# Optimization experiments

Hardware: AMD Instinct MI355X
Metric: run time of the kernel (lower is better)

The kernel has to match this reference:

```python
import jax, jax.numpy as jnp
import numpy as np

N = 100000      # num_nodes
E = 400000      # num edges
HID = 128       # hidden_channels (== in_channels, memory dim)
OUT = 64        # out_channels (per head)
HEADS = 4
HD = HEADS * OUT  # 256, TransformerConv concat output dim


def _lin(k, fan_in, fan_out):
    return jax.random.normal(k, (fan_in, fan_out), jnp.float32) * 0.02


def setup_inputs() -> dict:
    key = jax.random.key(0)
    ks = jax.random.split(key, 16)
    return {
        "edge_index": jax.random.randint(ks[0], (2, E), 0, N, dtype=jnp.int64),
        "edge_time": jax.random.randint(ks[1], (E, 1), 0, 1000000, dtype=jnp.int64),
        "x": jax.random.normal(ks[2], (N, HID), jnp.float32),
        "memory": jax.random.normal(ks[3], (N, HID), jnp.float32),  # TGN memory table (detached in fwd)
        # TransformerConv params (lin_query / lin_key / lin_value / lin_skip, all with bias)
        "Wq": _lin(ks[4], HID, HD), "bq": jnp.zeros((HD,), jnp.float32),
        "Wk": _lin(ks[5], HID, HD), "bk": jnp.zeros((HD,), jnp.float32),
        "Wv": _lin(ks[6], HID, HD), "bv": jnp.zeros((HD,), jnp.float32),
        "Wskip": _lin(ks[7], HID, HD), "bskip": jnp.zeros((HD,), jnp.float32),
        # rating MLP: Linear(512,128) -> ReLU -> Linear(128,64) -> ReLU -> Linear(64,1)
        "W1": _lin(ks[8], 2 * HD, 128), "b1": jnp.zeros((128,), jnp.float32),
        "W2": _lin(ks[9], 128, 64), "b2": jnp.zeros((64,), jnp.float32),
        "W3": _lin(ks[10], 64, 1), "b3": jnp.zeros((1,), jnp.float32),
    }


def reference(edge_index, edge_time, x, memory,
              Wq, bq, Wk, bk, Wv, bv, Wskip, bskip,
              W1, b1, W2, b2, W3, b3):
    src, dst = edge_index[0], edge_index[1]
    n = x.shape[0]

    # x = memory.detach() + x
    h = memory + x  # [N, HID]

    # TransformerConv (heads=4, concat=True, root_weight=True)
    q = (h @ Wq + bq).reshape(n, HEADS, OUT)
    k = (h @ Wk + bk).reshape(n, HEADS, OUT)
    v = (h @ Wv + bv).reshape(n, HEADS, OUT)

    # per-edge attention scores: messages flow src -> dst, softmax over in-edges of dst
    scores = jnp.sum(q[dst] * k[src], axis=-1) / jnp.sqrt(jnp.float32(OUT))  # [E, H]
    smax = jax.ops.segment_max(scores, dst, num_segments=n)                   # [N, H]
    e = jnp.exp(scores - smax[dst])
    denom = jax.ops.segment_sum(e, dst, num_segments=n)
    alpha = e / (denom[dst] + 1e-16)                                          # [E, H]

    agg = jax.ops.segment_sum(alpha[:, :, None] * v[src], dst, num_segments=n)  # [N, H, OUT]
    out = agg.reshape(n, HD) + (h @ Wskip + bskip)                              # skip connection

    # interaction embeddings + MLP head (dropout inactive at eval)
    inter = jnp.concatenate([out[src], out[dst]], axis=-1)  # [E, 512]
    hdd = jax.nn.relu(inter @ W1 + b1)
    hdd = jax.nn.relu(hdd @ W2 + b2)
    rating = jax.nn.sigmoid(hdd @ W3 + b3) * 4.0 + 1.0
    return rating[:, 0]
```

## Files before the change

kernel.cpp:

```cpp
#include <hip/hip_runtime.h>
#include <math.h>

#define N_NODES 100000
#define N_EDGES 400000
#define HID 128
#define HEADS 4
#define OUT_C 64
#define HD 256
#define SCAN_CHUNK 1024
#define NB_SCAN ((N_NODES + SCAN_CHUNK - 1) / SCAN_CHUNK)

typedef __attribute__((ext_vector_type(8))) short bf16x8;
typedef __attribute__((ext_vector_type(4))) float f32x4;

__device__ __forceinline__ unsigned short fbf(float f) {
    unsigned u = __float_as_uint(f);
    unsigned r = (u + 0x7fffu + ((u >> 16) & 1u)) >> 16;
    return (unsigned short)r;
}
__device__ __forceinline__ float bf2f(unsigned short u) {
    return __uint_as_float(((unsigned)u) << 16);
}

__device__ __forceinline__ void gl_lds16(const void* g, void* l) {
    __builtin_amdgcn_global_load_lds(
        (const __attribute__((address_space(1))) unsigned int*)g,
        (__attribute__((address_space(3))) unsigned int*)l,
        16, 0, 0);
}

__global__ __launch_bounds__(256) void init_zero(int* __restrict__ deg,
                                                 int* __restrict__ cursor) {
    int i = blockIdx.x * 256 + threadIdx.x;
    if (i < N_NODES) { deg[i] = 0; cursor[i] = 0; }
}

__global__ __launch_bounds__(256) void k_deg(const int* __restrict__ ei,
                                             int* __restrict__ deg) {
    int e = blockIdx.x * 256 + threadIdx.x;
    if (e < N_EDGES) atomicAdd(&deg[ei[N_EDGES + e]], 1);
}

__global__ __launch_bounds__(256) void k_scan1(const int* __restrict__ deg,
                                               int* __restrict__ rp,
                                               int* __restrict__ bsum) {
    __shared__ int ts[256];
    int b = blockIdx.x, t = threadIdx.x;
    int base = b * SCAN_CHUNK + t * 4;
    int vv[4];
    int s = 0;
#pragma unroll
    for (int i = 0; i < 4; ++i) {
        int d = (base + i < N_NODES) ? deg[base + i] : 0;
        vv[i] = s;
        s += d;
    }
    ts[t] = s;
    __syncthreads();
    for (int off = 1; off < 256; off <<= 1) {
        int x = (t >= off) ? ts[t - off] : 0;
        __syncthreads();
        ts[t] += x;
        __syncthreads();
    }
    int ex = ts[t] - s;
#pragma unroll
    for (int i = 0; i < 4; ++i)
        if (base + i < N_NODES) rp[base + i] = ex + vv[i];
    if (t == 255) bsum[b] = ts[255];
}

__global__ __launch_bounds__(256) void k_scan2(int* __restrict__ bsum) {
    __shared__ int ts[256];
    int t = threadIdx.x;
    int v = (t < NB_SCAN) ? bsum[t] : 0;
    ts[t] = v;
    __syncthreads();
    for (int off = 1; off < 256; off <<= 1) {
        int x = (t >= off) ? ts[t - off] : 0;
        __syncthreads();
        ts[t] += x;
        __syncthreads();
    }
    if (t < NB_SCAN) bsum[t] = ts[t] - v;
}

__global__ __launch_bounds__(256) void k_bucket(const int* __restrict__ ei,
                                                const int* __restrict__ rp,
                                                const int* __restrict__ bsum,
                                                int* __restrict__ cursor,
                                                int* __restrict__ csr_src,
                                                int* __restrict__ csr_dst,
                                                int* __restrict__ csr_eid) {
    int e = blockIdx.x * 256 + threadIdx.x;
    if (e >= N_EDGES) return;
    int src = ei[e];
    int d   = ei[N_EDGES + e];
    int idx = atomicAdd(&cursor[d], 1);
    int s   = rp[d] + bsum[d >> 10] + idx;
    csr_src[s] = src;
    csr_dst[s] = d;
    csr_eid[s] = e;
}

__global__ __launch_bounds__(256) void pack_all(
    const float* __restrict__ Wq, const float* __restrict__ Wk,
    const float* __restrict__ Wv, const float* __restrict__ Ws,
    const float* __restrict__ W1, const float* __restrict__ W2,
    unsigned short* __restrict__ Wp, unsigned short* __restrict__ Wcp,
    unsigned short* __restrict__ W2p) {
    int i = blockIdx.x * 256 + threadIdx.x;
    int lane = i & 63;
    int q = lane >> 4, c = lane & 15;
    if (i < 16384) {
        int nt = (i >> 6) & 15, kt = (i >> 10) & 3, z = i >> 12;
        const float* W = (z == 0) ? Wq : (z == 1) ? Wk : (z == 2) ? Wv : Ws;
#pragma unroll
        for (int j = 0; j < 8; ++j)
            Wp[i * 8 + j] = fbf(W[(kt * 32 + q * 8 + j) * HD + nt * 16 + c]);
    } else if (i < 24576) {
        int ii = i - 16384;
        int nt = (ii >> 6) & 15, kt = ii >> 10;
        int n = nt * 16 + c;
#pragma unroll
        for (int j = 0; j < 8; ++j) {
            int k = kt * 32 + q * 8 + j;
            float v = (n < 128) ? W1[k * 128 + n] : W1[(k + 256) * 128 + (n - 128)];
            Wcp[ii * 8 + j] = fbf(v);
        }
    } else if (i < 25600) {
        int ii = i - 24576;
        int nt = (ii >> 6) & 3, kt = ii >> 8;
#pragma unroll
        for (int j = 0; j < 8; ++j)
            W2p[ii * 8 + j] = fbf(W2[(kt * 32 + q * 8 + j) * 64 + nt * 16 + c]);
    }
}

__global__ __launch_bounds__(256) void k_pre(const float* __restrict__ x,
                                             const float* __restrict__ mem,
                                             unsigned short* __restrict__ H) {
    int idx = blockIdx.x * 256 + threadIdx.x;
    if (idx >= N_NODES * HID / 8) return;
    const float4* x4 = (const float4*)x;
    const float4* m4 = (const float4*)mem;
    float4 a0 = x4[(size_t)idx * 2],     a1 = x4[(size_t)idx * 2 + 1];
    float4 b0 = m4[(size_t)idx * 2],     b1 = m4[(size_t)idx * 2 + 1];
    bf16x8 hv;
    hv[0] = (short)fbf(a0.x + b0.x); hv[1] = (short)fbf(a0.y + b0.y);
    hv[2] = (short)fbf(a0.z + b0.z); hv[3] = (short)fbf(a0.w + b0.w);
    hv[4] = (short)fbf(a1.x + b1.x); hv[5] = (short)fbf(a1.y + b1.y);
    hv[6] = (short)fbf(a1.z + b1.z); hv[7] = (short)fbf(a1.w + b1.w);
    *(bf16x8*)&H[(size_t)idx * 8] = hv;
}

__global__ __launch_bounds__(256, 4) void gemm4(
    const unsigned short* __restrict__ H,
    const unsigned short* __restrict__ Wp,
    const float* __restrict__ bq, const float* __restrict__ bk,
    const float* __restrict__ bv, const float* __restrict__ bs,
    unsigned short* __restrict__ Q, unsigned short* __restrict__ KV,
    unsigned short* __restrict__ S)
{
    __shared__ __align__(16) short sh[4 * 64 * 68];
    short* As = sh;

    const int t = threadIdx.x;
    const int w = t >> 6, l = t & 63;
    const int q = l >> 4, c = l & 15;
    const int z  = blockIdx.y;
    const int m0 = blockIdx.x * 64;

#pragma unroll
    for (int i = 0; i < 4; ++i) {
        int rbase = w * 16 + i * 4;
        int r  = rbase + (l >> 4);
        int gr = m0 + r; if (gr >= N_NODES) gr = N_NODES - 1;
        int ks = (l & 15) ^ (r & 7);
        gl_lds16(&H[(size_t)gr * HID + ks * 8], &As[rbase * 128]);
    }

    const float* bz = (z == 0) ? bq : (z == 1) ? bk : (z == 2) ? bv : bs;
    float bb[4];
#pragma unroll
    for (int nt = 0; nt < 4; ++nt) bb[nt] = bz[w * 64 + nt * 16 + c];

    f32x4 acc[4][4];
#pragma unroll
    for (int mt = 0; mt < 4; ++mt)
#pragma unroll
        for (int nt = 0; nt < 4; ++nt) acc[mt][nt] = (f32x4){0.f, 0.f, 0.f, 0.f};

    __syncthreads();

#pragma unroll
    for (int kt = 0; kt < 4; ++kt) {
        bf16x8 af[4];
#pragma unroll
        for (int mt = 0; mt < 4; ++mt) {
            int row  = mt * 16 + c;
            int slot = (kt * 4 + q) ^ (row & 7);
            af[mt] = *(const bf16x8*)&As[row * 128 + slot * 8];
        }
#pragma unroll
        for (int nt = 0; nt < 4; ++nt) {
            bf16x8 bw8 = *(const bf16x8*)&Wp[(size_t)(((z * 4 + kt) * 16 + w * 4 + nt) * 64 + l) * 8];
#pragma unroll
            for (int mt = 0; mt < 4; ++mt)
                acc[mt][nt] = __builtin_amdgcn_mfma_f32_16x16x32_bf16(af[mt], bw8, acc[mt][nt], 0, 0, 0);
        }
    }
    __syncthreads();

    short* slab = &sh[w * 64 * 68];
#pragma unroll
    for (int nt = 0; nt < 4; ++nt)
#pragma unroll
        for (int mt = 0; mt < 4; ++mt)
#pragma unroll
            for (int r = 0; r < 4; ++r)
                slab[(mt * 16 + q * 4 + r) * 68 + nt * 16 + c] =
                    (short)fbf(acc[mt][nt][r] + bb[nt]);

    const int srow = l >> 3, schk = l & 7;
    if (z == 1 || z == 2) {
        const int voff = (z == 2) ? 4 : 0;
#pragma unroll
        for (int j = 0; j < 8; ++j) {
            int row = j * 8 + srow;
            int gr  = m0 + row;
            if (gr < N_NODES) {
                const short* sp = &slab[row * 68 + schk * 8];
                size_t base = (size_t)gr * 512 + w * 128 + schk * 16 + voff;
                *(ushort4*)&KV[base]     = *(const ushort4*)sp;
                *(ushort4*)&KV[base + 8] = *(const ushort4*)(sp + 4);
            }
        }
    } else {
        unsigned short* Oz = (z == 0) ? Q : S;
#pragma unroll
        for (int j = 0; j < 8; ++j) {
            int row = j * 8 + srow;
            int gr  = m0 + row;
            if (gr < N_NODES)
                *(bf16x8*)&Oz[(size_t)gr * HD + w * 64 + schk * 8] =
                    *(const bf16x8*)&slab[row * 68 + schk * 8];
        }
    }
}

__global__ __launch_bounds__(256) void k_attn(
    const int* __restrict__ rp, const int* __restrict__ bsum,
    const int* __restrict__ deg, const int* __restrict__ csr_src,
    const unsigned short* __restrict__ Q, const unsigned short* __restrict__ KV,
    const unsigned short* __restrict__ S,
    unsigned short* __restrict__ out)
{
    int node = blockIdx.x * 4 + (threadIdx.x >> 6);
    int l = threadIdx.x & 63;
    if (node >= N_NODES) return;
    int start = rp[node] + bsum[node >> 10];
    int cnt   = deg[node];

    float q0, q1, q2, q3;
    {
        ushort4 u = *(const ushort4*)&Q[(size_t)node * HD + l * 4];
        q0 = bf2f(u.x) * 0.125f; q1 = bf2f(u.y) * 0.125f;
        q2 = bf2f(u.z) * 0.125f; q3 = bf2f(u.w) * 0.125f;
    }

    float d = 0.f;
    float a0 = 0.f, a1 = 0.f, a2 = 0.f, a3 = 0.f;

    int i = 0;
    for (; i + 4 <= cnt; i += 4) {
        int s0 = csr_src[start + i];
        int s1 = csr_src[start + i + 1];
        int s2 = csr_src[start + i + 2];
        int s3 = csr_src[start + i + 3];
        bf16x8 k0 = *(const bf16x8*)&KV[(size_t)s0 * 512 + l * 8];
        bf16x8 k1 = *(const bf16x8*)&KV[(size_t)s1 * 512 + l * 8];
        bf16x8 k2 = *(const bf16x8*)&KV[(size_t)s2 * 512 + l * 8];
        bf16x8 k3 = *(const bf16x8*)&KV[(size_t)s3 * 512 + l * 8];
        float sA = q0 * bf2f((unsigned short)k0[0]) + q1 * bf2f((unsigned short)k0[1])
                 + q2 * bf2f((unsigned short)k0[2]) + q3 * bf2f((unsigned short)k0[3]);
        float sB = q0 * bf2f((unsigned short)k1[0]) + q1 * bf2f((unsigned short)k1[1])
                 + q2 * bf2f((unsigned short)k1[2]) + q3 * bf2f((unsigned short)k1[3]);
        float sC = q0 * bf2f((unsigned short)k2[0]) + q1 * bf2f((unsigned short)k2[1])
                 + q2 * bf2f((unsigned short)k2[2]) + q3 * bf2f((unsigned short)k2[3]);
        float sD = q0 * bf2f((unsigned short)k3[0]) + q1 * bf2f((unsigned short)k3[1])
                 + q2 * bf2f((unsigned short)k3[2]) + q3 * bf2f((unsigned short)k3[3]);
        sA += __shfl_xor(sA, 1); sB += __shfl_xor(sB, 1);
        sC += __shfl_xor(sC, 1); sD += __shfl_xor(sD, 1);
        sA += __shfl_xor(sA, 2); sB += __shfl_xor(sB, 2);
        sC += __shfl_xor(sC, 2); sD += __shfl_xor(sD, 2);
        sA += __shfl_xor(sA, 4); sB += __shfl_xor(sB, 4);
        sC += __shfl_xor(sC, 4); sD += __shfl_xor(sD, 4);
        sA += __shfl_xor(sA, 8); sB += __shfl_xor(sB, 8);
        sC += __shfl_xor(sC, 8); sD += __shfl_xor(sD, 8);
        float eA = __expf(sA), eB = __expf(sB), eC = __expf(sC), eD = __expf(sD);
        d += (eA + eB) + (eC + eD);
        a0 += eA * bf2f((unsigned short)k0[4]) + eB * bf2f((unsigned short)k1[4])
            + eC * bf2f((unsigned short)k2[4]) + eD * bf2f((unsigned short)k3[4]);
        a1 += eA * bf2f((unsigned short)k0[5]) + eB * bf2f((unsigned short)k1[5])
            + eC * bf2f((unsigned short)k2[5]) + eD * bf2f((unsigned short)k3[5]);
        a2 += eA * bf2f((unsigned short)k0[6]) + eB * bf2f((unsigned short)k1[6])
            + eC * bf2f((unsigned short)k2[6]) + eD * bf2f((unsigned short)k3[6]);
        a3 += eA * bf2f((unsigned short)k0[7]) + eB * bf2f((unsigned short)k1[7])
            + eC * bf2f((unsigned short)k2[7]) + eD * bf2f((unsigned short)k3[7]);
    }
    for (; i < cnt; ++i) {
        int s0 = csr_src[start + i];
        bf16x8 k0 = *(const bf16x8*)&KV[(size_t)s0 * 512 + l * 8];
        float sA = q0 * bf2f((unsigned short)k0[0]) + q1 * bf2f((unsigned short)k0[1])
                 + q2 * bf2f((unsigned short)k0[2]) + q3 * bf2f((unsigned short)k0[3]);
        sA += __shfl_xor(sA, 1);
        sA += __shfl_xor(sA, 2);
        sA += __shfl_xor(sA, 4);
        sA += __shfl_xor(sA, 8);
        float eA = __expf(sA);
        d += eA;
        a0 += eA * bf2f((unsigned short)k0[4]);
        a1 += eA * bf2f((unsigned short)k0[5]);
        a2 += eA * bf2f((unsigned short)k0[6]);
        a3 += eA * bf2f((unsigned short)k0[7]);
    }

    float inv = 1.f / (d + 1e-16f);
    ushort4 su = *(const ushort4*)&S[(size_t)node * HD + l * 4];
    ushort4 ov = make_ushort4(fbf(bf2f(su.x) + a0 * inv),
                              fbf(bf2f(su.y) + a1 * inv),
                              fbf(bf2f(su.z) + a2 * inv),
                              fbf(bf2f(su.w) + a3 * inv));
    *(ushort4*)&out[(size_t)node * HD + l * 4] = ov;
}

__global__ __launch_bounds__(256, 4) void pd_gemm(
    const unsigned short* __restrict__ outb,
    const unsigned short* __restrict__ Wcp,
    unsigned short* __restrict__ PD)
{
    __shared__ __align__(16) short sh[4 * 64 * 68];
    short* As = sh;

    const int t = threadIdx.x;
    const int w = t >> 6, l = t & 63;
    const int q = l >> 4, c = l & 15;
    const int m0 = blockIdx.x * 64;

#pragma unroll
    for (int i = 0; i < 8; ++i) {
        int rbase = w * 16 + i * 2;
        int r  = rbase + (l >> 5);
        int gr = m0 + r; if (gr >= N_NODES) gr = N_NODES - 1;
        int s  = (l & 31) ^ (r & 7);
        gl_lds16(&outb[(size_t)gr * HD + s * 8], &As[rbase * 256]);
    }

    f32x4 acc[4][4];
#pragma unroll
    for (int mt = 0; mt < 4; ++mt)
#pragma unroll
        for (int nt = 0; nt < 4; ++nt) acc[mt][nt] = (f32x4){0.f, 0.f, 0.f, 0.f};

    __syncthreads();

#pragma unroll
    for (int kt = 0; kt < 8; ++kt) {
        bf16x8 af[4];
#pragma unroll
        for (int mt = 0; mt < 4; ++mt) {
            int row  = mt * 16 + c;
            int slot = (kt * 4 + q) ^ (row & 7);
            af[mt] = *(const bf16x8*)&As[row * 256 + slot * 8];
        }
#pragma unroll
        for (int nt = 0; nt < 4; ++nt) {
            int ntg = w * 4 + nt;
            bf16x8 bv8 = *(const bf16x8*)&Wcp[(size_t)((kt * 16 + ntg) * 64 + l) * 8];
#pragma unroll
            for (int mt = 0; mt < 4; ++mt)
                acc[mt][nt] = __builtin_amdgcn_mfma_f32_16x16x32_bf16(af[mt], bv8, acc[mt][nt], 0, 0, 0);
        }
    }
    __syncthreads();

    short* slab = &sh[w * 64 * 68];
#pragma unroll
    for (int nt = 0; nt < 4; ++nt)
#pragma unroll
        for (int mt = 0; mt < 4; ++mt)
#pragma unroll
            for (int r = 0; r < 4; ++r)
                slab[(mt * 16 + q * 4 + r) * 68 + nt * 16 + c] =
                    (short)fbf(acc[mt][nt][r]);
    const int srow = l >> 3, schk = l & 7;
#pragma unroll
    for (int j = 0; j < 8; ++j) {
        int row = j * 8 + srow;
        int gr = m0 + row;
        if (gr < N_NODES)
            *(bf16x8*)&PD[(size_t)gr * HD + w * 64 + schk * 8] =
                *(const bf16x8*)&slab[row * 68 + schk * 8];
    }
}

__global__ __launch_bounds__(256) void edge_mlp_pd(
    const int* __restrict__ csr_src, const int* __restrict__ csr_dst,
    const int* __restrict__ csr_eid,
    const unsigned short* __restrict__ PD,
    const float* __restrict__ b1,
    const unsigned short* __restrict__ W2p, const float* __restrict__ b2,
    const float* __restrict__ W3, const float* __restrict__ b3,
    float* __restrict__ rating)
{
    __shared__ __align__(16) char lds[64 * 136 * 2];
    short* h1t = (short*)lds;
    float* h2s = (float*)lds;

    const int t = threadIdx.x;
    const int w = t >> 6, l = t & 63;
    const int q = l >> 4, c = l & 15;
    const int e0 = blockIdx.x * 64;

#pragma unroll
    for (int j = 0; j < 4; ++j) {
        int idx = t + j * 256;
        int row = idx >> 4, ch = idx & 15;
        int src = csr_src[e0 + row];
        int dst = csr_dst[e0 + row];
        bf16x8 pv = *(const bf16x8*)&PD[(size_t)src * HD + ch * 8];
        bf16x8 dv = *(const bf16x8*)&PD[(size_t)dst * HD + 128 + ch * 8];
        float4 ba = *(const float4*)&b1[ch * 8];
        float4 bb = *(const float4*)&b1[ch * 8 + 4];
        bf16x8 hv;
        hv[0] = (short)fbf(fmaxf(bf2f((unsigned short)pv[0]) + bf2f((unsigned short)dv[0]) + ba.x, 0.f));
        hv[1] = (short)fbf(fmaxf(bf2f((unsigned short)pv[1]) + bf2f((unsigned short)dv[1]) + ba.y, 0.f));
        hv[2] = (short)fbf(fmaxf(bf2f((unsigned short)pv[2]) + bf2f((unsigned short)dv[2]) + ba.z, 0.f));
        hv[3] = (short)fbf(fmaxf(bf2f((unsigned short)pv[3]) + bf2f((unsigned short)dv[3]) + ba.w, 0.f));
        hv[4] = (short)fbf(fmaxf(bf2f((unsigned short)pv[4]) + bf2f((unsigned short)dv[4]) + bb.x, 0.f));
        hv[5] = (short)fbf(fmaxf(bf2f((unsigned short)pv[5]) + bf2f((unsigned short)dv[5]) + bb.y, 0.f));
        hv[6] = (short)fbf(fmaxf(bf2f((unsigned short)pv[6]) + bf2f((unsigned short)dv[6]) + bb.z, 0.f));
        hv[7] = (short)fbf(fmaxf(bf2f((unsigned short)pv[7]) + bf2f((unsigned short)dv[7]) + bb.w, 0.f));
        *(bf16x8*)&h1t[row * 136 + ch * 8] = hv;
    }
    __syncthreads();

    f32x4 acc2[4];
#pragma unroll
    for (int i = 0; i < 4; ++i) acc2[i] = (f32x4){0.f, 0.f, 0.f, 0.f};
#pragma unroll
    for (int kt = 0; kt < 4; ++kt) {
        bf16x8 av = *(const bf16x8*)&h1t[(w * 16 + c) * 136 + kt * 32 + q * 8];
#pragma unroll
        for (int nt = 0; nt < 4; ++nt) {
            bf16x8 bv = *(const bf16x8*)&W2p[(size_t)((kt * 4 + nt) * 64 + l) * 8];
            acc2[nt] = __builtin_amdgcn_mfma_f32_16x16x32_bf16(av, bv, acc2[nt], 0, 0, 0);
        }
    }
    __syncthreads();

#pragma unroll
    for (int nt = 0; nt < 4; ++nt) {
        float bv = b2[nt * 16 + c];
#pragma unroll
        for (int r = 0; r < 4; ++r)
            h2s[(w * 16 + q * 4 + r) * 65 + nt * 16 + c] = fmaxf(acc2[nt][r] + bv, 0.f);
    }
    __syncthreads();

    if (t < 64) {
        float a = b3[0];
#pragma unroll 8
        for (int kk = 0; kk < 64; ++kk)
            a += h2s[t * 65 + kk] * W3[kk];
        rating[csr_eid[e0 + t]] = 4.f / (1.f + __expf(-a)) + 1.f;
    }
}

extern "C" void kernel_launch(void* const* d_in, const int* in_sizes, int n_in,
                              void* d_out, int out_size, void* d_ws, size_t ws_size,
                              hipStream_t stream) {
    const int*   ei  = (const int*)d_in[0];
    const float* x   = (const float*)d_in[2];
    const float* mem = (const float*)d_in[3];
    const float* Wq  = (const float*)d_in[4];
    const float* bq  = (const float*)d_in[5];
    const float* Wk  = (const float*)d_in[6];
    const float* bk  = (const float*)d_in[7];
    const float* Wv  = (const float*)d_in[8];
    const float* bv  = (const float*)d_in[9];
    const float* Ws  = (const float*)d_in[10];
    const float* bs  = (const float*)d_in[11];
    const float* W1  = (const float*)d_in[12];
    const float* b1  = (const float*)d_in[13];
    const float* W2  = (const float*)d_in[14];
    const float* b2  = (const float*)d_in[15];
    const float* W3  = (const float*)d_in[16];
    const float* b3  = (const float*)d_in[17];
    float* rating = (float*)d_out;

    unsigned short* Q = (unsigned short*)d_ws;
    const size_t NHDe = (size_t)N_NODES * HD;
    unsigned short* KV = Q + NHDe;
    unsigned short* S  = KV + 2 * NHDe;
    unsigned short* H  = S + NHDe;
    int* rp      = (int*)(H + (size_t)N_NODES * HID);
    int* deg     = rp + N_NODES;
    int* cursor  = deg + N_NODES;
    int* csr_src = cursor + N_NODES;
    int* csr_dst = csr_src + N_EDGES;
    int* csr_eid = csr_dst + N_EDGES;
    int* bsum    = csr_eid + N_EDGES;
    unsigned short* Wp  = (unsigned short*)(bsum + 128);
    unsigned short* Wcp = Wp + 16384 * 8;
    unsigned short* W2p = Wcp + 8192 * 8;
    unsigned short* PD  = KV;

    const int nblk  = (N_NODES + 255) / 256;
    const int eblk  = (N_EDGES + 255) / 256;
    const int wgrid = (N_NODES + 3) / 4;
    const int pblk  = (N_NODES * HID / 8 + 255) / 256;

    init_zero<<<nblk, 256, 0, stream>>>(deg, cursor);
    k_deg<<<eblk, 256, 0, stream>>>(ei, deg);
    k_scan1<<<NB_SCAN, 256, 0, stream>>>(deg, rp, bsum);
    k_scan2<<<1, 256, 0, stream>>>(bsum);
    k_bucket<<<eblk, 256, 0, stream>>>(ei, rp, bsum, cursor, csr_src, csr_dst, csr_eid);
    pack_all<<<100, 256, 0, stream>>>(Wq, Wk, Wv, Ws, W1, W2, Wp, Wcp, W2p);

    k_pre<<<pblk, 256, 0, stream>>>(x, mem, H);

    gemm4<<<dim3((N_NODES + 63) / 64, 4), dim3(256), 0, stream>>>(
        H, Wp, bq, bk, bv, bs, Q, KV, S);

    k_attn<<<wgrid, 256, 0, stream>>>(rp, bsum, deg, csr_src, Q, KV, S, Q);

    pd_gemm<<<(N_NODES + 63) / 64, 256, 0, stream>>>(Q, Wcp, PD);

    edge_mlp_pd<<<N_EDGES / 64, 256, 0, stream>>>(
        csr_src, csr_dst, csr_eid, PD, b1, W2p, b2, W3, b3, rating);
}
```

Before: 456.3 us.

## Compute two projections per GEMM block, interleave K/V writes, tweak attention tail

```diff
diff --git a/kernel.cpp b/kernel.cpp
--- a/kernel.cpp
+++ b/kernel.cpp
@@ -9,6 +9,7 @@
 #define HD 256
 #define SCAN_CHUNK 1024
 #define NB_SCAN ((N_NODES + SCAN_CHUNK - 1) / SCAN_CHUNK)
+#define SLAB_STRIDE 4356
 
 typedef __attribute__((ext_vector_type(8))) short bf16x8;
 typedef __attribute__((ext_vector_type(4))) float f32x4;
@@ -27,12 +28,6 @@
         (const __attribute__((address_space(1))) unsigned int*)g,
         (__attribute__((address_space(3))) unsigned int*)l,
         16, 0, 0);
-}
-
-__global__ __launch_bounds__(256) void init_zero(int* __restrict__ deg,
-                                                 int* __restrict__ cursor) {
-    int i = blockIdx.x * 256 + threadIdx.x;
-    if (i < N_NODES) { deg[i] = 0; cursor[i] = 0; }
 }
 
 __global__ __launch_bounds__(256) void k_deg(const int* __restrict__ ei,
@@ -154,7 +149,57 @@
     *(bf16x8*)&H[(size_t)idx * 8] = hv;
 }
 
-__global__ __launch_bounds__(256, 4) void gemm4(
+__device__ __forceinline__ void mfma_pass(f32x4 acc[4][4], const short* As,
+        const unsigned short* __restrict__ Wp, int z, int w, int l, int q, int c) {
+#pragma unroll
+    for (int mt = 0; mt < 4; ++mt)
+#pragma unroll
+        for (int nt = 0; nt < 4; ++nt) acc[mt][nt] = (f32x4){0.f, 0.f, 0.f, 0.f};
+#pragma unroll
+    for (int kt = 0; kt < 4; ++kt) {
+        bf16x8 af[4];
+#pragma unroll
+        for (int mt = 0; mt < 4; ++mt) {
+            int row  = mt * 16 + c;
+            int slot = (kt * 4 + q) ^ (row & 7);
+            af[mt] = *(const bf16x8*)&As[row * 128 + slot * 8];
+        }
+#pragma unroll
+        for (int nt = 0; nt < 4; ++nt) {
+            bf16x8 bw8 = *(const bf16x8*)&Wp[(size_t)(((z * 4 + kt) * 16 + w * 4 + nt) * 64 + l) * 8];
+#pragma unroll
+            for (int mt = 0; mt < 4; ++mt)
+                acc[mt][nt] = __builtin_amdgcn_mfma_f32_16x16x32_bf16(af[mt], bw8, acc[mt][nt], 0, 0, 0);
+        }
+    }
+}
+
+__device__ __forceinline__ void slab_store(short* slab, const f32x4 acc[4][4],
+        const float bb[4], int q, int c) {
+#pragma unroll
+    for (int nt = 0; nt < 4; ++nt)
+#pragma unroll
+        for (int mt = 0; mt < 4; ++mt)
+#pragma unroll
+            for (int r = 0; r < 4; ++r)
+                slab[(mt * 16 + q * 4 + r) * 68 + nt * 16 + c] =
+                    (short)fbf(acc[mt][nt][r] + bb[nt]);
+}
+
+__device__ __forceinline__ void store_rows(unsigned short* __restrict__ O,
+        const short* slab, int m0, int w, int l) {
+    const int srow = l >> 3, schk = l & 7;
+#pragma unroll
+    for (int j = 0; j < 8; ++j) {
+        int row = j * 8 + srow;
+        int gr  = m0 + row;
+        if (gr < N_NODES)
+            *(bf16x8*)&O[(size_t)gr * HD + w * 64 + schk * 8] =
+                *(const bf16x8*)&slab[row * 68 + schk * 8];
+    }
+}
+
+__global__ __launch_bounds__(256, 3) void gemm4(
     const unsigned short* __restrict__ H,
     const unsigned short* __restrict__ Wp,
     const float* __restrict__ bq, const float* __restrict__ bk,
@@ -162,13 +207,13 @@
     unsigned short* __restrict__ Q, unsigned short* __restrict__ KV,
     unsigned short* __restrict__ S)
 {
-    __shared__ __align__(16) short sh[4 * 64 * 68];
-    short* As = sh;
+    __shared__ __align__(16) short As[64 * 128];
+    __shared__ __align__(16) short Slab[4 * SLAB_STRIDE];
 
     const int t = threadIdx.x;
     const int w = t >> 6, l = t & 63;
     const int q = l >> 4, c = l & 15;
-    const int z  = blockIdx.y;
+    const int y  = blockIdx.y;
     const int m0 = blockIdx.x * 64;
 
 #pragma unroll
@@ -180,71 +225,55 @@
         gl_lds16(&H[(size_t)gr * HID + ks * 8], &As[rbase * 128]);
     }
 
-    const float* bz = (z == 0) ? bq : (z == 1) ? bk : (z == 2) ? bv : bs;
-    float bb[4];
-#pragma unroll
-    for (int nt = 0; nt < 4; ++nt) bb[nt] = bz[w * 64 + nt * 16 + c];
-
+    const int   zA  = (y == 0) ? 0 : 1;
+    const int   zB  = (y == 0) ? 3 : 2;
+    const float* bA = (y == 0) ? bq : bk;
+    const float* bB = (y == 0) ? bs : bv;
+    float bbA[4], bbB[4];
+#pragma unroll
+    for (int nt = 0; nt < 4; ++nt) {
+        bbA[nt] = bA[w * 64 + nt * 16 + c];
+        bbB[nt] = bB[w * 64 + nt * 16 + c];
+    }
+
+    __syncthreads();
+
+    short* slab = &Slab[w * SLAB_STRIDE];
     f32x4 acc[4][4];
-#pragma unroll
-    for (int mt = 0; mt < 4; ++mt)
-#pragma unroll
-        for (int nt = 0; nt < 4; ++nt) acc[mt][nt] = (f32x4){0.f, 0.f, 0.f, 0.f};
-
-    __syncthreads();
-
-#pragma unroll
-    for (int kt = 0; kt < 4; ++kt) {
-        bf16x8 af[4];
-#pragma unroll
-        for (int mt = 0; mt < 4; ++mt) {
-            int row  = mt * 16 + c;
-            int slot = (kt * 4 + q) ^ (row & 7);
-            af[mt] = *(const bf16x8*)&As[row * 128 + slot * 8];
-        }
-#pragma unroll
-        for (int nt = 0; nt < 4; ++nt) {
-            bf16x8 bw8 = *(const bf16x8*)&Wp[(size_t)(((z * 4 + kt) * 16 + w * 4 + nt) * 64 + l) * 8];
-#pragma unroll
-            for (int mt = 0; mt < 4; ++mt)
-                acc[mt][nt] = __builtin_amdgcn_mfma_f32_16x16x32_bf16(af[mt], bw8, acc[mt][nt], 0, 0, 0);
-        }
-    }
-    __syncthreads();
-
-    short* slab = &sh[w * 64 * 68];
-#pragma unroll
-    for (int nt = 0; nt < 4; ++nt)
-#pragma unroll
-        for (int mt = 0; mt < 4; ++mt)
-#pragma unroll
-            for (int r = 0; r < 4; ++r)
-                slab[(mt * 16 + q * 4 + r) * 68 + nt * 16 + c] =
-                    (short)fbf(acc[mt][nt][r] + bb[nt]);
-
-    const int srow = l >> 3, schk = l & 7;
-    if (z == 1 || z == 2) {
-        const int voff = (z == 2) ? 4 : 0;
-#pragma unroll
-        for (int j = 0; j < 8; ++j) {
-            int row = j * 8 + srow;
-            int gr  = m0 + row;
+    ushort4 kreg[16];
+    const int koff = (l & 15) * 4;
+    const short* cslab = &Slab[(l >> 4) * SLAB_STRIDE];
+
+    mfma_pass(acc, As, Wp, zA, w, l, q, c);
+    slab_store(slab, acc, bbA, q, c);
+    if (y == 0) {
+        store_rows(Q, slab, m0, w, l);
+    } else {
+        __syncthreads();
+#pragma unroll
+        for (int i = 0; i < 16; ++i)
+            kreg[i] = *(const ushort4*)&cslab[(w * 16 + i) * 68 + koff];
+        __syncthreads();
+    }
+
+    mfma_pass(acc, As, Wp, zB, w, l, q, c);
+    slab_store(slab, acc, bbB, q, c);
+    if (y == 0) {
+        store_rows(S, slab, m0, w, l);
+    } else {
+        __syncthreads();
+#pragma unroll
+        for (int i = 0; i < 16; ++i) {
+            int gr = m0 + w * 16 + i;
+            ushort4 vr = *(const ushort4*)&cslab[(w * 16 + i) * 68 + koff];
             if (gr < N_NODES) {
-                const short* sp = &slab[row * 68 + schk * 8];
-                size_t base = (size_t)gr * 512 + w * 128 + schk * 16 + voff;
-                *(ushort4*)&KV[base]     = *(const ushort4*)sp;
-                *(ushort4*)&KV[base + 8] = *(const ushort4*)(sp + 4);
+                bf16x8 ov;
+                ov[0] = (short)kreg[i].x; ov[1] = (short)kreg[i].y;
+                ov[2] = (short)kreg[i].z; ov[3] = (short)kreg[i].w;
+                ov[4] = (short)vr.x;      ov[5] = (short)vr.y;
+                ov[6] = (short)vr.z;      ov[7] = (short)vr.w;
+                *(bf16x8*)&KV[(size_t)gr * 512 + l * 8] = ov;
             }
-        }
-    } else {
-        unsigned short* Oz = (z == 0) ? Q : S;
-#pragma unroll
-        for (int j = 0; j < 8; ++j) {
-            int row = j * 8 + srow;
-            int gr  = m0 + row;
-            if (gr < N_NODES)
-                *(bf16x8*)&Oz[(size_t)gr * HD + w * 64 + schk * 8] =
-                    *(const bf16x8*)&slab[row * 68 + schk * 8];
         }
     }
 }
@@ -309,7 +338,28 @@
         a3 += eA * bf2f((unsigned short)k0[7]) + eB * bf2f((unsigned short)k1[7])
             + eC * bf2f((unsigned short)k2[7]) + eD * bf2f((unsigned short)k3[7]);
     }
-    for (; i < cnt; ++i) {
+    if (i + 2 <= cnt) {
+        int s0 = csr_src[start + i];
+        int s1 = csr_src[start + i + 1];
+        bf16x8 k0 = *(const bf16x8*)&KV[(size_t)s0 * 512 + l * 8];
+        bf16x8 k1 = *(const bf16x8*)&KV[(size_t)s1 * 512 + l * 8];
+        float sA = q0 * bf2f((unsigned short)k0[0]) + q1 * bf2f((unsigned short)k0[1])
+                 + q2 * bf2f((unsigned short)k0[2]) + q3 * bf2f((unsigned short)k0[3]);
+        float sB = q0 * bf2f((unsigned short)k1[0]) + q1 * bf2f((unsigned short)k1[1])
+                 + q2 * bf2f((unsigned short)k1[2]) + q3 * bf2f((unsigned short)k1[3]);
+        sA += __shfl_xor(sA, 1); sB += __shfl_xor(sB, 1);
+        sA += __shfl_xor(sA, 2); sB += __shfl_xor(sB, 2);
+        sA += __shfl_xor(sA, 4); sB += __shfl_xor(sB, 4);
+        sA += __shfl_xor(sA, 8); sB += __shfl_xor(sB, 8);
+        float eA = __expf(sA), eB = __expf(sB);
+        d += eA + eB;
+        a0 += eA * bf2f((unsigned short)k0[4]) + eB * bf2f((unsigned short)k1[4]);
+        a1 += eA * bf2f((unsigned short)k0[5]) + eB * bf2f((unsigned short)k1[5]);
+        a2 += eA * bf2f((unsigned short)k0[6]) + eB * bf2f((unsigned short)k1[6]);
+        a3 += eA * bf2f((unsigned short)k0[7]) + eB * bf2f((unsigned short)k1[7]);
+        i += 2;
+    }
+    if (i < cnt) {
         int s0 = csr_src[start + i];
         bf16x8 k0 = *(const bf16x8*)&KV[(size_t)s0 * 512 + l * 8];
         float sA = q0 * bf2f((unsigned short)k0[0]) + q1 * bf2f((unsigned short)k0[1])
@@ -517,12 +567,11 @@
     unsigned short* W2p = Wcp + 8192 * 8;
     unsigned short* PD  = KV;
 
-    const int nblk  = (N_NODES + 255) / 256;
     const int eblk  = (N_EDGES + 255) / 256;
     const int wgrid = (N_NODES + 3) / 4;
     const int pblk  = (N_NODES * HID / 8 + 255) / 256;
 
-    init_zero<<<nblk, 256, 0, stream>>>(deg, cursor);
+    hipMemsetAsync(deg, 0, sizeof(int) * 2 * N_NODES, stream);
     k_deg<<<eblk, 256, 0, stream>>>(ei, deg);
     k_scan1<<<NB_SCAN, 256, 0, stream>>>(deg, rp, bsum);
     k_scan2<<<1, 256, 0, stream>>>(bsum);
@@ -531,7 +580,7 @@
 
     k_pre<<<pblk, 256, 0, stream>>>(x, mem, H);
 
-    gemm4<<<dim3((N_NODES + 63) / 64, 4), dim3(256), 0, stream>>>(
+    gemm4<<<dim3((N_NODES + 63) / 64, 2), dim3(256), 0, stream>>>(
         H, Wp, bq, bk, bv, bs, Q, KV, S);
 
     k_attn<<<wgrid, 256, 0, stream>>>(rp, bsum, deg, csr_src, Q, KV, S, Q);
```

After: 422.7 us. 7.4% less time.
